# Kernel optimization log

Measured on AMD Instinct MI355X. Metric: run time of the kernel, lower is better.

## Reference

```python
import jax, jax.numpy as jnp
import numpy as np
from itertools import combinations

# 2-source PID on the redundancy lattice (Williams-Beer), antichains indexed
# over sources {0,1}; index 2 is the output variable axis.
FULL = (0, 1, 2)
ANTICHAINS = [((0,), (1,)), ((0,),), ((1,),), ((0, 1),)]  # red, unq0, unq1, syn (cumulative I)
MOEBIUS = np.array([[1, 0, 0, 0],
                    [-1, 1, 0, 0],
                    [-1, 0, 1, 0],
                    [1, -1, -1, 1]], dtype=np.float32)
EPS_DEN = 1e-10
EPS_FRAC = 1e-7


def _marginals(p):
    """Powerset marginals of the joint p over axes (0,1,2); trailing axis = neurons."""
    m = {}
    for r in range(1, 4):
        for a in combinations(FULL, r):
            ax = tuple(sorted(set(FULL) - set(a)))
            m[a] = p.sum(ax, keepdims=True) if ax else p
    return m


def _union(m, alpha):
    """Inclusion-exclusion union probability over the sets in antichain alpha."""
    res = 0.0
    for k in range(1, len(alpha) + 1):
        for beta in combinations(alpha, k):
            b_union = tuple(sorted({b for a in beta for b in a}))
            res = res + ((-1) ** (k - 1)) * m[b_union]
    return res


def _isx(m, alpha, p_full):
    """I_cap^sx for one antichain: sum over joint of p * log2 ratio."""
    p_union = jax.lax.stop_gradient(_union(m, alpha))            # no_grad in original
    alpha_t = tuple(tuple(sorted(a + (2,))) for a in alpha)       # append output var
    p_union_t = _union(m, alpha_t)
    frac = p_union_t / (p_union * m[(2,)] + EPS_DEN)
    frac = jnp.where(frac < EPS_FRAC, jnp.asarray(1.0, frac.dtype), frac)
    return (p_full * jnp.log2(frac)).sum((0, 1, 2))               # -> (N,)


def _pid(p):
    m = _marginals(p)
    I_cap = jnp.stack([_isx(m, a, p) for a in ANTICHAINS])        # (4, N)
    Pi = jnp.asarray(MOEBIUS, p.dtype) @ I_cap                    # Moebius transform (4, N)
    p_out = m[(2,)]                                               # (1, 1, out_bins, N)
    H_tot = -(p_out * jnp.log2(p_out + EPS_DEN)).sum(-2)          # (1, 1, N)
    H_res = (H_tot - I_cap[ANTICHAINS.index(((0, 1),))]).reshape(-1)
    return jnp.concatenate([Pi, H_res[None]], axis=0)             # (5, N): red,unq0,unq1,syn,H_res


def setup_inputs() -> dict:
    key = jax.random.key(0)
    # joint histogram over (src1_bins=16, src2_bins=16, out_bins=2, n_neurons=100000)
    p = jax.random.uniform(key, (16, 16, 2, 100000), dtype=jnp.float32)
    p = p / p.sum((0, 1, 2), keepdims=True)  # normalize to a distribution per neuron
    return {"p_all_neurons": p}


def reference(p_all_neurons):
    return _pid(p_all_neurons)
```

## Files before the change

kernel.cpp:

```cpp
#include <hip/hip_runtime.h>

#define LOG2_EPS_CLAMP -23.2534966f

__device__ __forceinline__ float flog2(float x) { return __builtin_amdgcn_logf(x); }

__global__ __launch_bounds__(256, 5) void pid_kernel(const float* __restrict__ p,
                                                     float* __restrict__ out,
                                                     const int N) {
    const int tid = threadIdx.x;
    const int s = (tid >> 3) & 7;
    const int g = (tid & 7) + ((tid >> 6) << 3);
    const int n = blockIdx.x * 32 + g;
    if (n >= N) return;
    const float* __restrict__ q = p + n;

    float m12p[32];
    #pragma unroll
    for (int t = 0; t < 32; ++t) m12p[t] = 0.f;
    float a0[2], a1[2];

    #pragma unroll
    for (int ii = 0; ii < 2; ++ii) {
        const int i = s * 2 + ii;
        const float* __restrict__ qi = q + (size_t)(i * 32) * (size_t)N;
        float s0 = 0.f, s1 = 0.f;
        #pragma unroll
        for (int j = 0; j < 16; ++j) {
            const float f0 = qi[(size_t)(2 * j) * (size_t)N];
            const float f1 = qi[(size_t)(2 * j + 1) * (size_t)N];
            s0 += f0; s1 += f1;
            m12p[2 * j]     += f0;
            m12p[2 * j + 1] += f1;
        }
        a0[ii] = s0; a1[ii] = s1;
    }

    #pragma unroll
    for (int t = 0; t < 32; ++t) {
        m12p[t] += __shfl_xor(m12p[t], 8, 64);
        m12p[t] += __shfl_xor(m12p[t], 16, 64);
        m12p[t] += __shfl_xor(m12p[t], 32, 64);
    }

    float P20 = 0.f, P21 = 0.f;
    #pragma unroll
    for (int j = 0; j < 16; ++j) { P20 += m12p[2 * j]; P21 += m12p[2 * j + 1]; }
    const float LP20 = flog2(P20);
    const float LP21 = flog2(P21);

    float I1 = 0.f, I2 = 0.f, I4 = 0.f;
    #pragma unroll
    for (int ii = 0; ii < 2; ++ii) {
        const int i = s * 2 + ii;
        const float a0i = a0[ii], a1i = a1[ii];
        const float m0i = a0i + a1i;
        const float* __restrict__ qi = q + (size_t)(i * 32) * (size_t)N;
        #pragma unroll
        for (int j = 0; j < 16; ++j) {
            const float f0  = qi[(size_t)(2 * j) * (size_t)N];
            const float f1  = qi[(size_t)(2 * j + 1) * (size_t)N];
            const float p01 = f0 + f1;
            const float m1j = m12p[2 * j] + m12p[2 * j + 1];
            const float u1  = m0i + m1j - p01;
            const float Lu1  = flog2(u1);
            const float Lp01 = flog2(p01);
            {
                const float num = a0i + m12p[2 * j] - f0;
                float l1 = flog2(num) - Lu1 - LP20;
                l1 = (l1 < LOG2_EPS_CLAMP) ? 0.f : l1;
                I1 = fmaf(f0, l1, I1);
                float l4 = flog2(f0) - Lp01 - LP20;
                l4 = (l4 < LOG2_EPS_CLAMP) ? 0.f : l4;
                I4 = fmaf(f0, l4, I4);
            }
            {
                const float num = a1i + m12p[2 * j + 1] - f1;
                float l1 = flog2(num) - Lu1 - LP21;
                l1 = (l1 < LOG2_EPS_CLAMP) ? 0.f : l1;
                I1 = fmaf(f1, l1, I1);
                float l4 = flog2(f1) - Lp01 - LP21;
                l4 = (l4 < LOG2_EPS_CLAMP) ? 0.f : l4;
                I4 = fmaf(f1, l4, I4);
            }
        }
        const float L0 = flog2(m0i);
        float la = flog2(a0i) - L0 - LP20;
        la = (la < LOG2_EPS_CLAMP) ? 0.f : la;
        I2 = fmaf(a0i, la, I2);
        float lb = flog2(a1i) - L0 - LP21;
        lb = (lb < LOG2_EPS_CLAMP) ? 0.f : lb;
        I2 = fmaf(a1i, lb, I2);
    }

    I1 += __shfl_xor(I1, 8, 64); I1 += __shfl_xor(I1, 16, 64); I1 += __shfl_xor(I1, 32, 64);
    I2 += __shfl_xor(I2, 8, 64); I2 += __shfl_xor(I2, 16, 64); I2 += __shfl_xor(I2, 32, 64);
    I4 += __shfl_xor(I4, 8, 64); I4 += __shfl_xor(I4, 16, 64); I4 += __shfl_xor(I4, 32, 64);

    float I3 = 0.f;
    #pragma unroll
    for (int j = 0; j < 16; ++j) {
        const float L1 = flog2(m12p[2 * j] + m12p[2 * j + 1]);
        float la = flog2(m12p[2 * j]) - L1 - LP20;
        la = (la < LOG2_EPS_CLAMP) ? 0.f : la;
        I3 = fmaf(m12p[2 * j], la, I3);
        float lb = flog2(m12p[2 * j + 1]) - L1 - LP21;
        lb = (lb < LOG2_EPS_CLAMP) ? 0.f : lb;
        I3 = fmaf(m12p[2 * j + 1], lb, I3);
    }

    const float H = -(P20 * flog2(P20 + 1e-10f) + P21 * flog2(P21 + 1e-10f));

    if (s == 0) {
        out[0 * N + n] = I1;
        out[1 * N + n] = I2 - I1;
        out[2 * N + n] = I3 - I1;
        out[3 * N + n] = I1 - I2 - I3 + I4;
        out[4 * N + n] = H - I4;
    }
}

extern "C" void kernel_launch(void* const* d_in, const int* in_sizes, int n_in,
                              void* d_out, int out_size, void* d_ws, size_t ws_size,
                              hipStream_t stream) {
    const float* p = (const float*)d_in[0];
    float* out = (float*)d_out;
    const int N = in_sizes[0] / 512;
    const int blocks = (N + 31) / 32;
    pid_kernel<<<blocks, 256, 0, stream>>>(p, out, N);
}
```

Measured before the change: 328.3 us.

## Split each neuron across 16 threads, one source row per thread

The thread mapping changes from 8 threads per neuron with two rows of the first source each to 16 threads per neuron with one row each. Blocks now cover 16 neurons instead of 32 and the occupancy hint in launch bounds is removed. The goal is more parallelism and fewer live registers per thread for this memory-bound reduction. In exchange, coalescing drops to runs of 4 neurons (16 bytes) per wavefront segment, there is one extra shuffle stage per reduction, and the redundant I3 tail computation is repeated by more threads.

```diff
diff --git a/kernel.cpp b/kernel.cpp
--- a/kernel.cpp
+++ b/kernel.cpp
@@ -4,39 +4,32 @@
 
 __device__ __forceinline__ float flog2(float x) { return __builtin_amdgcn_logf(x); }
 
-__global__ __launch_bounds__(256, 5) void pid_kernel(const float* __restrict__ p,
-                                                     float* __restrict__ out,
-                                                     const int N) {
+__global__ __launch_bounds__(256) void pid_kernel(const float* __restrict__ p,
+                                                  float* __restrict__ out,
+                                                  const int N) {
     const int tid = threadIdx.x;
-    const int s = (tid >> 3) & 7;
-    const int g = (tid & 7) + ((tid >> 6) << 3);
-    const int n = blockIdx.x * 32 + g;
+    const int s = (tid >> 2) & 15;
+    const int g = (tid & 3) + ((tid >> 6) << 2);
+    const int n = blockIdx.x * 16 + g;
     if (n >= N) return;
     const float* __restrict__ q = p + n;
+    const float* __restrict__ qi = q + (size_t)(s * 32) * (size_t)N;
 
     float m12p[32];
-    #pragma unroll
-    for (int t = 0; t < 32; ++t) m12p[t] = 0.f;
-    float a0[2], a1[2];
+    float a0 = 0.f, a1 = 0.f;
 
     #pragma unroll
-    for (int ii = 0; ii < 2; ++ii) {
-        const int i = s * 2 + ii;
-        const float* __restrict__ qi = q + (size_t)(i * 32) * (size_t)N;
-        float s0 = 0.f, s1 = 0.f;
-        #pragma unroll
-        for (int j = 0; j < 16; ++j) {
-            const float f0 = qi[(size_t)(2 * j) * (size_t)N];
-            const float f1 = qi[(size_t)(2 * j + 1) * (size_t)N];
-            s0 += f0; s1 += f1;
-            m12p[2 * j]     += f0;
-            m12p[2 * j + 1] += f1;
-        }
-        a0[ii] = s0; a1[ii] = s1;
+    for (int j = 0; j < 16; ++j) {
+        const float f0 = qi[(size_t)(2 * j) * (size_t)N];
+        const float f1 = qi[(size_t)(2 * j + 1) * (size_t)N];
+        a0 += f0; a1 += f1;
+        m12p[2 * j]     = f0;
+        m12p[2 * j + 1] = f1;
     }
 
     #pragma unroll
     for (int t = 0; t < 32; ++t) {
+        m12p[t] += __shfl_xor(m12p[t], 4, 64);
         m12p[t] += __shfl_xor(m12p[t], 8, 64);
         m12p[t] += __shfl_xor(m12p[t], 16, 64);
         m12p[t] += __shfl_xor(m12p[t], 32, 64);
@@ -48,53 +41,53 @@
     const float LP20 = flog2(P20);
     const float LP21 = flog2(P21);
 
-    float I1 = 0.f, I2 = 0.f, I4 = 0.f;
+    float I1 = 0.f, I4 = 0.f;
+    const float m0i = a0 + a1;
     #pragma unroll
-    for (int ii = 0; ii < 2; ++ii) {
-        const int i = s * 2 + ii;
-        const float a0i = a0[ii], a1i = a1[ii];
-        const float m0i = a0i + a1i;
-        const float* __restrict__ qi = q + (size_t)(i * 32) * (size_t)N;
-        #pragma unroll
-        for (int j = 0; j < 16; ++j) {
-            const float f0  = qi[(size_t)(2 * j) * (size_t)N];
-            const float f1  = qi[(size_t)(2 * j + 1) * (size_t)N];
-            const float p01 = f0 + f1;
-            const float m1j = m12p[2 * j] + m12p[2 * j + 1];
-            const float u1  = m0i + m1j - p01;
-            const float Lu1  = flog2(u1);
-            const float Lp01 = flog2(p01);
-            {
-                const float num = a0i + m12p[2 * j] - f0;
-                float l1 = flog2(num) - Lu1 - LP20;
-                l1 = (l1 < LOG2_EPS_CLAMP) ? 0.f : l1;
-                I1 = fmaf(f0, l1, I1);
-                float l4 = flog2(f0) - Lp01 - LP20;
-                l4 = (l4 < LOG2_EPS_CLAMP) ? 0.f : l4;
-                I4 = fmaf(f0, l4, I4);
-            }
-            {
-                const float num = a1i + m12p[2 * j + 1] - f1;
-                float l1 = flog2(num) - Lu1 - LP21;
-                l1 = (l1 < LOG2_EPS_CLAMP) ? 0.f : l1;
-                I1 = fmaf(f1, l1, I1);
-                float l4 = flog2(f1) - Lp01 - LP21;
-                l4 = (l4 < LOG2_EPS_CLAMP) ? 0.f : l4;
-                I4 = fmaf(f1, l4, I4);
-            }
+    for (int j = 0; j < 16; ++j) {
+        const float f0  = qi[(size_t)(2 * j) * (size_t)N];
+        const float f1  = qi[(size_t)(2 * j + 1) * (size_t)N];
+        const float p01 = f0 + f1;
+        const float m1j = m12p[2 * j] + m12p[2 * j + 1];
+        const float u1  = m0i + m1j - p01;
+        const float Lu1  = flog2(u1);
+        const float Lp01 = flog2(p01);
+        {
+            const float num = a0 + m12p[2 * j] - f0;
+            float l1 = flog2(num) - Lu1 - LP20;
+            l1 = (l1 < LOG2_EPS_CLAMP) ? 0.f : l1;
+            I1 = fmaf(f0, l1, I1);
+            float l4 = flog2(f0) - Lp01 - LP20;
+            l4 = (l4 < LOG2_EPS_CLAMP) ? 0.f : l4;
+            I4 = fmaf(f0, l4, I4);
         }
-        const float L0 = flog2(m0i);
-        float la = flog2(a0i) - L0 - LP20;
-        la = (la < LOG2_EPS_CLAMP) ? 0.f : la;
-        I2 = fmaf(a0i, la, I2);
-        float lb = flog2(a1i) - L0 - LP21;
-        lb = (lb < LOG2_EPS_CLAMP) ? 0.f : lb;
-        I2 = fmaf(a1i, lb, I2);
+        {
+            const float num = a1 + m12p[2 * j + 1] - f1;
+            float l1 = flog2(num) - Lu1 - LP21;
+            l1 = (l1 < LOG2_EPS_CLAMP) ? 0.f : l1;
+            I1 = fmaf(f1, l1, I1);
+            float l4 = flog2(f1) - Lp01 - LP21;
+            l4 = (l4 < LOG2_EPS_CLAMP) ? 0.f : l4;
+            I4 = fmaf(f1, l4, I4);
+        }
     }
 
-    I1 += __shfl_xor(I1, 8, 64); I1 += __shfl_xor(I1, 16, 64); I1 += __shfl_xor(I1, 32, 64);
-    I2 += __shfl_xor(I2, 8, 64); I2 += __shfl_xor(I2, 16, 64); I2 += __shfl_xor(I2, 32, 64);
-    I4 += __shfl_xor(I4, 8, 64); I4 += __shfl_xor(I4, 16, 64); I4 += __shfl_xor(I4, 32, 64);
+    float I2;
+    {
+        const float L0 = flog2(m0i);
+        float la = flog2(a0) - L0 - LP20;
+        la = (la < LOG2_EPS_CLAMP) ? 0.f : la;
+        float lb = flog2(a1) - L0 - LP21;
+        lb = (lb < LOG2_EPS_CLAMP) ? 0.f : lb;
+        I2 = a0 * la + a1 * lb;
+    }
+
+    #pragma unroll
+    for (int m = 4; m <= 32; m <<= 1) {
+        I1 += __shfl_xor(I1, m, 64);
+        I2 += __shfl_xor(I2, m, 64);
+        I4 += __shfl_xor(I4, m, 64);
+    }
 
     float I3 = 0.f;
     #pragma unroll
@@ -125,6 +118,6 @@
     const float* p = (const float*)d_in[0];
     float* out = (float*)d_out;
     const int N = in_sizes[0] / 512;
-    const int blocks = (N + 31) / 32;
+    const int blocks = (N + 15) / 16;
     pid_kernel<<<blocks, 256, 0, stream>>>(p, out, N);
 }
```

New measurement: 308.0 us. 1.07x faster.
